# Kernel tuning notes

Measured on AMD Instinct MI355X. Metric: run time of the kernel, lower is better.

The kernel has to match this reference:

```python
import jax, jax.numpy as jnp
import numpy as np
import math

B, S, D_MODEL, H = 2, 2048, 1024, 16
D_HEAD = D_MODEL // H
THETA = 10000.0


def _init_linear(key, out_f, in_f):
    std = math.sqrt(2.0 / (out_f + in_f))
    w = jax.random.truncated_normal(key, -3.0, 3.0, (out_f, in_f), dtype=jnp.float32)
    return w * std


def setup_inputs() -> dict:
    key = jax.random.key(0)
    k1, k2, k3 = jax.random.split(key, 3)
    x = jax.random.normal(k1, (B, S, D_MODEL), dtype=jnp.float32)
    wqkv = _init_linear(k2, 3 * D_MODEL, D_MODEL)
    w_out = _init_linear(k3, D_MODEL, D_MODEL)
    # RoPE tables: positions [max_seq_len,1] * inv_freq [d_head//2]
    positions = jnp.arange(S, dtype=jnp.float32)[:, None]
    freqs = jnp.arange(0, D_HEAD, 2, dtype=jnp.float32) / D_HEAD
    inv_freq = 1.0 / (THETA ** freqs)
    angles = positions * inv_freq  # [S, D_HEAD//2]
    cos = jnp.cos(angles)
    sin = jnp.sin(angles)
    token_positions = jnp.arange(S, dtype=jnp.int32)
    return {"x": x, "wqkv": wqkv, "w_out": w_out, "cos": cos, "sin": sin,
            "token_positions": token_positions}


def _apply_rope(t, cos_pos, sin_pos):
    # t: [b, h, s, d], cos/sin_pos: [s, d//2] broadcast over b,h
    te = t[..., 0::2]
    to = t[..., 1::2]
    re = te * cos_pos - to * sin_pos
    ro = te * sin_pos + to * cos_pos
    # interleave even/odd back: [..., d//2, 2] -> [..., d]
    out = jnp.stack([re, ro], axis=-1)
    return out.reshape(t.shape)


def reference(x, wqkv, w_out, cos, sin, token_positions):
    b, s, d_model = x.shape
    qkv = jnp.einsum('oi,bsi->bso', wqkv, x)  # [b, s, 3*d_model]
    q, k, v = jnp.split(qkv, 3, axis=-1)

    def to_heads(t):
        return t.reshape(b, s, H, D_HEAD).transpose(0, 2, 1, 3)  # b h s d

    q, k, v = to_heads(q), to_heads(k), to_heads(v)

    cos_pos = cos[token_positions]  # [s, d_head//2]
    sin_pos = sin[token_positions]
    q = _apply_rope(q, cos_pos, sin_pos)
    k = _apply_rope(k, cos_pos, sin_pos)

    scores = jnp.einsum('bhqd,bhkd->bhqk', q, k) / math.sqrt(D_HEAD)
    causal = jnp.tril(jnp.ones((s, s), dtype=bool))  # ~triu(diag=1)
    scores = jnp.where(causal, scores, -jnp.inf)
    weights = jax.nn.softmax(scores, axis=-1)
    y = jnp.einsum('bhqk,bhkd->bhqd', weights, v)
    y = y.transpose(0, 2, 1, 3).reshape(b, s, d_model)
    return jnp.einsum('oi,bsi->bso', w_out, y)
```

## Files before the change

### kernel.cpp

```cpp
#include <hip/hip_runtime.h>
#include <hip/hip_bf16.h>


#define S_LEN 2048
#define DMODEL 1024
#define NH 16
#define QKVN 3072

typedef __attribute__((ext_vector_type(4))) short short4v;
typedef __attribute__((ext_vector_type(8))) short short8v;
typedef __attribute__((ext_vector_type(4))) float floatx4;

#define CSOFT 0.18033688f

__device__ __forceinline__ unsigned short f2bf(float f) {
  unsigned int u = __float_as_uint(f);
  u += 0x7FFFu + ((u >> 16) & 1u);
  return (unsigned short)(u >> 16);
}
__device__ __forceinline__ float bf2f(unsigned short u) {
  return __uint_as_float(((unsigned int)u) << 16);
}
__device__ __forceinline__ void gload16(const void* g, void* l) {
  __builtin_amdgcn_global_load_lds((const __attribute__((address_space(1))) void*)g,
                                   (__attribute__((address_space(3))) void*)l,
                                   16, 0, 0);
}
__device__ __forceinline__ int perm4(int c) {
  return (c >> 3) * 32 + (c & 3) * 8 + ((c >> 2) & 1) * 4;
}

__global__ __launch_bounds__(256) void cast_bf16_perm_k(const float* __restrict__ in,
                                                        unsigned short* __restrict__ out,
                                                        int nchunk) {
  int i = blockIdx.x * 256 + threadIdx.x;
  if (i >= nchunk) return;
  int c = i & 3;
  const float4* f4 = reinterpret_cast<const float4*>(in);
  float4 lo = f4[(i >> 2) * 8 + c];
  float4 hi = f4[(i >> 2) * 8 + 4 + c];
  short8v o;
  o[0] = (short)f2bf(lo.x); o[1] = (short)f2bf(lo.y);
  o[2] = (short)f2bf(lo.z); o[3] = (short)f2bf(lo.w);
  o[4] = (short)f2bf(hi.x); o[5] = (short)f2bf(hi.y);
  o[6] = (short)f2bf(hi.z); o[7] = (short)f2bf(hi.w);
  reinterpret_cast<short8v*>(out)[i] = o;
}

template <bool OUT_BF16>
__global__ __launch_bounds__(256) void gemm_bt(const unsigned short* __restrict__ A,
                                               const unsigned short* __restrict__ Bm,
                                               void* __restrict__ Cp, int M, int N, int K) {
  __shared__ __align__(16) unsigned short As[2][128 * 32];
  __shared__ __align__(16) unsigned short Bs[2][128 * 32];
  const int tid = threadIdx.x;
  const int lane = tid & 63;
  const int w = tid >> 6;
  const int wm = w >> 1, wn = w & 1;
  const int l15 = lane & 15, l4 = lane >> 4;
  const int bm = blockIdx.y * 128, bn = blockIdx.x * 128;
  const int srow = lane >> 2;
  const int schunk = ((lane & 3) - ((lane >> 3) & 3)) & 3;
  const int rslot = (l4 + (l15 >> 1)) & 3;

  floatx4 acc[4][4] = {};
  const int nt = K >> 5;

#define GSTAGE(T, BUF)                                                                   \
  {                                                                                      \
    const int k0s = (T) << 5;                                                            \
    _Pragma("unroll") for (int j = 0; j < 2; ++j) {                                      \
      const unsigned short* ga =                                                         \
          A + (size_t)(bm + j * 64 + w * 16 + srow) * K + k0s + schunk * 8;              \
      gload16(ga, &As[BUF][j * 2048 + w * 512]);                                         \
      const unsigned short* gb =                                                         \
          Bm + (size_t)(bn + j * 64 + w * 16 + srow) * K + k0s + schunk * 8;             \
      gload16(gb, &Bs[BUF][j * 2048 + w * 512]);                                         \
    }                                                                                    \
  }

  GSTAGE(0, 0);
  for (int t = 0; t < nt; ++t) {
    const int cur = t & 1;
    if (t + 1 < nt) {
      GSTAGE(t + 1, cur ^ 1);
      asm volatile("s_waitcnt vmcnt(4)" ::: "memory");
    } else {
      asm volatile("s_waitcnt vmcnt(0)" ::: "memory");
    }
    __syncthreads();

    short8v af[4], bfr[4];
#pragma unroll
    for (int f = 0; f < 4; ++f) {
      af[f]  = *(const short8v*)(&As[cur][(wm * 64 + f * 16 + l15) * 32 + rslot * 8]);
      bfr[f] = *(const short8v*)(&Bs[cur][(wn * 64 + f * 16 + l15) * 32 + rslot * 8]);
    }
#pragma unroll
    for (int f = 0; f < 4; ++f)
#pragma unroll
      for (int g = 0; g < 4; ++g)
        acc[f][g] = __builtin_amdgcn_mfma_f32_16x16x32_bf16(af[f], bfr[g], acc[f][g], 0, 0, 0);
    __syncthreads();
  }
#undef GSTAGE

#pragma unroll
  for (int f = 0; f < 4; ++f)
#pragma unroll
    for (int g = 0; g < 4; ++g)
#pragma unroll
      for (int r = 0; r < 4; ++r) {
        int row = bm + wm * 64 + f * 16 + l4 * 4 + r;
        int col = bn + wn * 64 + g * 16 + l15;
        if (OUT_BF16)
          ((unsigned short*)Cp)[(size_t)row * N + col] = f2bf(acc[f][g][r]);
        else
          ((float*)Cp)[(size_t)row * N + col] = acc[f][g][r];
      }
}

__global__ __launch_bounds__(256) void rope_pack_k(const unsigned short* __restrict__ qkvb,
                                                   unsigned short* __restrict__ qp_,
                                                   unsigned short* __restrict__ kp_,
                                                   unsigned short* __restrict__ vtp_,
                                                   const float* __restrict__ cosp,
                                                   const float* __restrict__ sinp,
                                                   const int* __restrict__ tpos) {
  __shared__ unsigned short Vs[64][68];
  const int tid = threadIdx.x;
  const int bh = blockIdx.x >> 5;
  const int st = blockIdx.x & 31;
  const int b = bh >> 4, h = bh & 15;
  const int c = tid & 15, t0 = tid >> 4;
  const int s0 = st * 64;
  const int pc = perm4(c);

#pragma unroll
  for (int it = 0; it < 4; ++it) {
    const int tl = it * 16 + t0;
    const int s = s0 + tl;
    const int tp = tpos[s];
    const size_t base = ((size_t)(b * S_LEN + s)) * QKVN + h * 64 + c * 4;
    const float co0 = cosp[tp * 32 + 2 * c], si0 = sinp[tp * 32 + 2 * c];
    const float co1 = cosp[tp * 32 + 2 * c + 1], si1 = sinp[tp * 32 + 2 * c + 1];
    {
      const float c0 = co0 * CSOFT, s0q = si0 * CSOFT;
      const float c1 = co1 * CSOFT, s1q = si1 * CSOFT;
      ushort4 rv = *(const ushort4*)(qkvb + base);
      float a0 = bf2f(rv.x), a1 = bf2f(rv.y), a2 = bf2f(rv.z), a3 = bf2f(rv.w);
      ushort4 ov;
      ov.x = f2bf(a0 * c0 - a1 * s0q); ov.y = f2bf(a0 * s0q + a1 * c0);
      ov.z = f2bf(a2 * c1 - a3 * s1q); ov.w = f2bf(a2 * s1q + a3 * c1);
      *(ushort4*)(qp_ + ((size_t)bh * S_LEN + s) * 64 + pc) = ov;
    }
    {
      ushort4 rv = *(const ushort4*)(qkvb + base + DMODEL);
      float a0 = bf2f(rv.x), a1 = bf2f(rv.y), a2 = bf2f(rv.z), a3 = bf2f(rv.w);
      ushort4 ov;
      ov.x = f2bf(a0 * co0 - a1 * si0); ov.y = f2bf(a0 * si0 + a1 * co0);
      ov.z = f2bf(a2 * co1 - a3 * si1); ov.w = f2bf(a2 * si1 + a3 * co1);
      *(ushort4*)(kp_ + ((size_t)bh * S_LEN + s) * 64 + pc) = ov;
    }
    {
      ushort4 rv = *(const ushort4*)(qkvb + base + 2 * DMODEL);
      *(ushort4*)(&Vs[tl][c * 4]) = rv;
    }
  }
  __syncthreads();
#pragma unroll
  for (int it = 0; it < 4; ++it) {
    const int d = it * 16 + t0;
    ushort4 ov;
    ov.x = Vs[c * 4 + 0][d]; ov.y = Vs[c * 4 + 1][d];
    ov.z = Vs[c * 4 + 2][d]; ov.w = Vs[c * 4 + 3][d];
    *(ushort4*)(vtp_ + ((size_t)bh * 64 + d) * S_LEN + s0 + pc) = ov;
  }
}

__device__ __forceinline__ short8v readfrag128(const unsigned short* L, int row, int cc) {
  return *(const short8v*)(L + row * 64 + (((cc) ^ (row & 7)) << 3));
}

__device__ __forceinline__ void stage_tiles(const unsigned short* kg0, const unsigned short* vg0,
                                            int kt, unsigned short* Kb, unsigned short* Vb,
                                            int tid, int w) {
#pragma unroll
  for (int i = 0; i < 2; ++i) {
    int jj = i * 256 + tid;
    int row = jj >> 3;
    int cc = (jj & 7) ^ (row & 7);
    gload16(kg0 + (size_t)kt * 4096 + row * 64 + cc * 8, Kb + (i * 256 + w * 64) * 8);
    gload16(vg0 + (size_t)row * S_LEN + kt * 64 + cc * 8, Vb + (i * 256 + w * 64) * 8);
  }
}

__global__ __launch_bounds__(256) void attn_mfma(const unsigned short* __restrict__ qp_,
                                                 const unsigned short* __restrict__ kp_,
                                                 const unsigned short* __restrict__ vtp_,
                                                 unsigned short* __restrict__ yb) {
  __shared__ __align__(16) unsigned short Kl[2][4096];
  __shared__ __align__(16) unsigned short Vl[2][4096];
  const int tid = threadIdx.x;
  const int lane = tid & 63, w = tid >> 6;
  const int l15 = lane & 15, l4 = lane >> 4;
  const int j = blockIdx.x;
  const int bh = (j & 7) + 8 * ((j >> 3) & 3);
  const int qt = 31 - (j >> 5);
  const int b = bh >> 4, h = bh & 15;

  const unsigned short* kg0 = kp_ + (size_t)bh * S_LEN * 64;
  const unsigned short* vg0 = vtp_ + (size_t)bh * 64 * S_LEN;

  const unsigned short* qp = qp_ + ((size_t)bh * S_LEN + qt * 64 + w * 16 + l15) * 64;
  short8v qf[2];
#pragma unroll
  for (int c2 = 0; c2 < 2; ++c2)
    qf[c2] = *(const short8v*)(qp + c2 * 32 + l4 * 8);

  floatx4 o[4] = {};
  float mrun = -1e30f, lsum = 0.f;

  stage_tiles(kg0, vg0, 0, Kl[0], Vl[0], tid, w);

  for (int kt = 0; kt <= qt; ++kt) {
    const int cur = kt & 1;
    if (kt < qt) {
      stage_tiles(kg0, vg0, kt + 1, Kl[cur ^ 1], Vl[cur ^ 1], tid, w);
      asm volatile("s_waitcnt vmcnt(4)" ::: "memory");
    } else {
      asm volatile("s_waitcnt vmcnt(0)" ::: "memory");
    }
    __syncthreads();

    const unsigned short* Kc = Kl[cur];
    const unsigned short* Vc = Vl[cur];
    const bool diag = (kt == qt);
    float s_[4][4];
    __builtin_amdgcn_s_setprio(1);
#pragma unroll
    for (int g = 0; g < 4; ++g) {
      if (diag && g > w) {
        s_[g][0] = s_[g][1] = s_[g][2] = s_[g][3] = -INFINITY;
        continue;
      }
      short8v k0 = readfrag128(Kc, g * 16 + l15, l4);
      short8v k1 = readfrag128(Kc, g * 16 + l15, 4 + l4);
      floatx4 t = {0.f, 0.f, 0.f, 0.f};
      t = __builtin_amdgcn_mfma_f32_16x16x32_bf16(k0, qf[0], t, 0, 0, 0);
      t = __builtin_amdgcn_mfma_f32_16x16x32_bf16(k1, qf[1], t, 0, 0, 0);
#pragma unroll
      for (int r = 0; r < 4; ++r) {
        float v = t[r];
        if (diag && g == w && (l4 * 4 + r > l15)) v = -INFINITY;
        s_[g][r] = v;
      }
    }
    __builtin_amdgcn_s_setprio(0);

    float tm = -INFINITY;
#pragma unroll
    for (int g = 0; g < 4; ++g)
#pragma unroll
      for (int r = 0; r < 4; ++r) tm = fmaxf(tm, s_[g][r]);
    tm = fmaxf(tm, __shfl_xor(tm, 16));
    tm = fmaxf(tm, __shfl_xor(tm, 32));

    if (!__all(tm <= mrun + 3.0f)) {
      float nm = fmaxf(mrun, tm);
      float rs = exp2f(mrun - nm);
      mrun = nm;
      lsum *= rs;
      float rsr[4];
#pragma unroll
      for (int r = 0; r < 4; ++r) rsr[r] = __shfl(rs, l4 * 4 + r);
#pragma unroll
      for (int dt = 0; dt < 4; ++dt)
#pragma unroll
        for (int r = 0; r < 4; ++r) o[dt][r] *= rsr[r];
    }

    union { unsigned short u[16]; short8v v[2]; } pk;
    float psum = 0.f;
#pragma unroll
    for (int g = 0; g < 4; ++g)
#pragma unroll
      for (int r = 0; r < 4; ++r) {
        float p = exp2f(s_[g][r] - mrun);
        psum += p;
        pk.u[g * 4 + r] = (unsigned short)(__float_as_uint(p) >> 16);
      }
    lsum += psum;

    __builtin_amdgcn_s_setprio(1);
#pragma unroll
    for (int dt = 0; dt < 4; ++dt) {
      short8v v0 = readfrag128(Vc, dt * 16 + l15, l4);
      short8v v1 = readfrag128(Vc, dt * 16 + l15, 4 + l4);
      o[dt] = __builtin_amdgcn_mfma_f32_16x16x32_bf16(pk.v[0], v0, o[dt], 0, 0, 0);
      o[dt] = __builtin_amdgcn_mfma_f32_16x16x32_bf16(pk.v[1], v1, o[dt], 0, 0, 0);
    }
    __builtin_amdgcn_s_setprio(0);
    __syncthreads();
  }

  lsum += __shfl_xor(lsum, 16);
  lsum += __shfl_xor(lsum, 32);
  float linv = 1.f / lsum;
  float lr[4];
#pragma unroll
  for (int r = 0; r < 4; ++r) lr[r] = __shfl(linv, l4 * 4 + r);
#pragma unroll
  for (int dt = 0; dt < 4; ++dt)
#pragma unroll
    for (int r = 0; r < 4; ++r) {
      size_t row = (size_t)(b * S_LEN + qt * 64 + w * 16 + l4 * 4 + r);
      int col = (h * 2 + (dt >> 1)) * 32 + (l15 >> 2) * 8 + (l15 & 3) + 4 * (dt & 1);
      yb[row * DMODEL + col] = f2bf(o[dt][r] * lr[r]);
    }
}

extern "C" void kernel_launch(void* const* d_in, const int* in_sizes, int n_in,
                              void* d_out, int out_size, void* d_ws, size_t ws_size,
                              hipStream_t stream) {
  const float* x     = (const float*)d_in[0];
  const float* wqkv  = (const float*)d_in[1];
  const float* w_out = (const float*)d_in[2];
  const float* cosp  = (const float*)d_in[3];
  const float* sinp  = (const float*)d_in[4];
  const int*   tpos  = (const int*)d_in[5];
  float* out = (float*)d_out;
  char* ws = (char*)d_ws;

  const size_t MB = 1024 * 1024;
  unsigned short* xb    = (unsigned short*)(ws + 0);
  unsigned short* wqkvb = (unsigned short*)(ws + 8 * MB);
  unsigned short* wob   = (unsigned short*)(ws + 14 * MB);
  unsigned short* qkvb  = (unsigned short*)(ws + 16 * MB);
  unsigned short* qpk   = (unsigned short*)(ws + 40 * MB);
  unsigned short* kpk   = (unsigned short*)(ws + 48 * MB);
  unsigned short* vtpk  = (unsigned short*)(ws + 56 * MB);
  unsigned short* yb    = (unsigned short*)(ws + 0);

  cast_bf16_perm_k<<<2048, 256, 0, stream>>>(x, xb, 524288);
  cast_bf16_perm_k<<<1536, 256, 0, stream>>>(wqkv, wqkvb, 393216);
  cast_bf16_perm_k<<<512, 256, 0, stream>>>(w_out, wob, 131072);

  gemm_bt<true><<<dim3(24, 32), 256, 0, stream>>>(xb, wqkvb, qkvb, 4096, QKVN, 1024);

  rope_pack_k<<<1024, 256, 0, stream>>>(qkvb, qpk, kpk, vtpk, cosp, sinp, tpos);

  attn_mfma<<<1024, 256, 0, stream>>>(qpk, kpk, vtpk, yb);

  gemm_bt<false><<<dim3(8, 32), 256, 0, stream>>>(yb, wob, out, 4096, DMODEL, 1024);
}
```

Measured before the change: 197.5 us.

## Unroll GEMM and attention loops by two, compute softmax row sums via MFMA

Both the GEMM main loop and the attention KV loop are manually unrolled by two, so the double-buffer index becomes a compile-time constant and the per-iteration buffer-select arithmetic goes away. In attention, the row sum of the probabilities is now produced by an MFMA against a ones vector rather than by scalar adds plus cross-lane shuffles. This sums the bf16-truncated probabilities, so the normaliser matches the values fed to the PV product. The rescale threshold is raised from 3 to 8, so the lazy rescale is skipped more often, at the cost of larger unnormalised accumulators. The GEMM unroll assumes an even K-tile count, which holds for K=1024.

New measurement: 198.1 us. About the same (+0.3%).

```diff
diff --git a/kernel.cpp b/kernel.cpp
--- a/kernel.cpp
+++ b/kernel.cpp
@@ -79,30 +79,32 @@
     }                                                                                    \
   }
 
+#define GBODY(T, BUF)                                                                    \
+  {                                                                                      \
+    if ((T) + 1 < nt) {                                                                  \
+      GSTAGE((T) + 1, BUF ^ 1);                                                          \
+      asm volatile("s_waitcnt vmcnt(4)" ::: "memory");                                   \
+    } else {                                                                             \
+      asm volatile("s_waitcnt vmcnt(0)" ::: "memory");                                   \
+    }                                                                                    \
+    __syncthreads();                                                                     \
+    short8v af[4], bfr[4];                                                               \
+    _Pragma("unroll") for (int f = 0; f < 4; ++f) {                                      \
+      af[f]  = *(const short8v*)(&As[BUF][(wm * 64 + f * 16 + l15) * 32 + rslot * 8]);   \
+      bfr[f] = *(const short8v*)(&Bs[BUF][(wn * 64 + f * 16 + l15) * 32 + rslot * 8]);   \
+    }                                                                                    \
+    _Pragma("unroll") for (int f = 0; f < 4; ++f)                                        \
+      _Pragma("unroll") for (int g = 0; g < 4; ++g)                                      \
+        acc[f][g] = __builtin_amdgcn_mfma_f32_16x16x32_bf16(af[f], bfr[g], acc[f][g], 0, 0, 0); \
+    __syncthreads();                                                                     \
+  }
+
   GSTAGE(0, 0);
-  for (int t = 0; t < nt; ++t) {
-    const int cur = t & 1;
-    if (t + 1 < nt) {
-      GSTAGE(t + 1, cur ^ 1);
-      asm volatile("s_waitcnt vmcnt(4)" ::: "memory");
-    } else {
-      asm volatile("s_waitcnt vmcnt(0)" ::: "memory");
-    }
-    __syncthreads();
-
-    short8v af[4], bfr[4];
-#pragma unroll
-    for (int f = 0; f < 4; ++f) {
-      af[f]  = *(const short8v*)(&As[cur][(wm * 64 + f * 16 + l15) * 32 + rslot * 8]);
-      bfr[f] = *(const short8v*)(&Bs[cur][(wn * 64 + f * 16 + l15) * 32 + rslot * 8]);
-    }
-#pragma unroll
-    for (int f = 0; f < 4; ++f)
-#pragma unroll
-      for (int g = 0; g < 4; ++g)
-        acc[f][g] = __builtin_amdgcn_mfma_f32_16x16x32_bf16(af[f], bfr[g], acc[f][g], 0, 0, 0);
-    __syncthreads();
-  }
+  for (int t = 0; t < nt; t += 2) {
+    GBODY(t, 0);
+    GBODY(t + 1, 1);
+  }
+#undef GBODY
 #undef GSTAGE
 
 #pragma unroll
@@ -218,105 +220,101 @@
   for (int c2 = 0; c2 < 2; ++c2)
     qf[c2] = *(const short8v*)(qp + c2 * 32 + l4 * 8);
 
+  const short8v ones8 = {(short)0x3F80, (short)0x3F80, (short)0x3F80, (short)0x3F80,
+                         (short)0x3F80, (short)0x3F80, (short)0x3F80, (short)0x3F80};
+
   floatx4 o[4] = {};
-  float mrun = -1e30f, lsum = 0.f;
+  floatx4 ls = {0.f, 0.f, 0.f, 0.f};
+  float mrun = -1e30f;
+
+#define ATTN_BODY(KT, BUF)                                                             \
+  {                                                                                    \
+    const int kt_ = (KT);                                                              \
+    if (kt_ < qt) {                                                                    \
+      stage_tiles(kg0, vg0, kt_ + 1, Kl[BUF ^ 1], Vl[BUF ^ 1], tid, w);                \
+      asm volatile("s_waitcnt vmcnt(4)" ::: "memory");                                 \
+    } else {                                                                           \
+      asm volatile("s_waitcnt vmcnt(0)" ::: "memory");                                 \
+    }                                                                                  \
+    __syncthreads();                                                                   \
+    const bool diag = (kt_ == qt);                                                     \
+    float s_[4][4];                                                                    \
+    __builtin_amdgcn_s_setprio(1);                                                     \
+    _Pragma("unroll") for (int g = 0; g < 4; ++g) {                                    \
+      if (diag && g > w) {                                                             \
+        s_[g][0] = s_[g][1] = s_[g][2] = s_[g][3] = -INFINITY;                         \
+        continue;                                                                      \
+      }                                                                                \
+      short8v k0 = readfrag128(Kl[BUF], g * 16 + l15, l4);                             \
+      short8v k1 = readfrag128(Kl[BUF], g * 16 + l15, 4 + l4);                         \
+      floatx4 t = {0.f, 0.f, 0.f, 0.f};                                                \
+      t = __builtin_amdgcn_mfma_f32_16x16x32_bf16(k0, qf[0], t, 0, 0, 0);              \
+      t = __builtin_amdgcn_mfma_f32_16x16x32_bf16(k1, qf[1], t, 0, 0, 0);              \
+      _Pragma("unroll") for (int r = 0; r < 4; ++r) {                                  \
+        float v = t[r];                                                                \
+        if (diag && g == w && (l4 * 4 + r > l15)) v = -INFINITY;                       \
+        s_[g][r] = v;                                                                  \
+      }                                                                                \
+    }                                                                                  \
+    __builtin_amdgcn_s_setprio(0);                                                     \
+    float tm = fmaxf(fmaxf(s_[0][0], s_[0][1]), s_[0][2]);                             \
+    tm = fmaxf(fmaxf(tm, s_[0][3]), s_[1][0]);                                         \
+    tm = fmaxf(fmaxf(tm, s_[1][1]), s_[1][2]);                                         \
+    tm = fmaxf(fmaxf(tm, s_[1][3]), s_[2][0]);                                         \
+    tm = fmaxf(fmaxf(tm, s_[2][1]), s_[2][2]);                                         \
+    tm = fmaxf(fmaxf(tm, s_[2][3]), s_[3][0]);                                         \
+    tm = fmaxf(fmaxf(tm, s_[3][1]), s_[3][2]);                                         \
+    tm = fmaxf(tm, s_[3][3]);                                                          \
+    tm = fmaxf(tm, __shfl_xor(tm, 16));                                                \
+    tm = fmaxf(tm, __shfl_xor(tm, 32));                                                \
+    if (!__all(tm <= mrun + 8.0f)) {                                                   \
+      float nm = fmaxf(mrun, tm);                                                      \
+      float rs = exp2f(mrun - nm);                                                     \
+      mrun = nm;                                                                       \
+      float rsr[4];                                                                    \
+      _Pragma("unroll") for (int r = 0; r < 4; ++r) rsr[r] = __shfl(rs, l4 * 4 + r);   \
+      _Pragma("unroll") for (int r = 0; r < 4; ++r) ls[r] *= rsr[r];                   \
+      _Pragma("unroll") for (int dt = 0; dt < 4; ++dt)                                 \
+        _Pragma("unroll") for (int r = 0; r < 4; ++r) o[dt][r] *= rsr[r];              \
+    }                                                                                  \
+    union { unsigned short u[16]; short8v v[2]; } pk;                                  \
+    _Pragma("unroll") for (int g = 0; g < 4; ++g)                                      \
+      _Pragma("unroll") for (int r = 0; r < 4; ++r) {                                  \
+        float p = exp2f(s_[g][r] - mrun);                                              \
+        pk.u[g * 4 + r] = (unsigned short)(__float_as_uint(p) >> 16);                  \
+      }                                                                                \
+    __builtin_amdgcn_s_setprio(1);                                                     \
+    ls = __builtin_amdgcn_mfma_f32_16x16x32_bf16(pk.v[0], ones8, ls, 0, 0, 0);         \
+    ls = __builtin_amdgcn_mfma_f32_16x16x32_bf16(pk.v[1], ones8, ls, 0, 0, 0);         \
+    _Pragma("unroll") for (int dt = 0; dt < 4; ++dt) {                                 \
+      short8v v0 = readfrag128(Vl[BUF], dt * 16 + l15, l4);                            \
+      short8v v1 = readfrag128(Vl[BUF], dt * 16 + l15, 4 + l4);                        \
+      o[dt] = __builtin_amdgcn_mfma_f32_16x16x32_bf16(pk.v[0], v0, o[dt], 0, 0, 0);    \
+      o[dt] = __builtin_amdgcn_mfma_f32_16x16x32_bf16(pk.v[1], v1, o[dt], 0, 0, 0);    \
+    }                                                                                  \
+    __builtin_amdgcn_s_setprio(0);                                                     \
+    __syncthreads();                                                                   \
+  }
 
   stage_tiles(kg0, vg0, 0, Kl[0], Vl[0], tid, w);
-
-  for (int kt = 0; kt <= qt; ++kt) {
-    const int cur = kt & 1;
-    if (kt < qt) {
-      stage_tiles(kg0, vg0, kt + 1, Kl[cur ^ 1], Vl[cur ^ 1], tid, w);
-      asm volatile("s_waitcnt vmcnt(4)" ::: "memory");
-    } else {
-      asm volatile("s_waitcnt vmcnt(0)" ::: "memory");
-    }
-    __syncthreads();
-
-    const unsigned short* Kc = Kl[cur];
-    const unsigned short* Vc = Vl[cur];
-    const bool diag = (kt == qt);
-    float s_[4][4];
-    __builtin_amdgcn_s_setprio(1);
-#pragma unroll
-    for (int g = 0; g < 4; ++g) {
-      if (diag && g > w) {
-        s_[g][0] = s_[g][1] = s_[g][2] = s_[g][3] = -INFINITY;
-        continue;
-      }
-      short8v k0 = readfrag128(Kc, g * 16 + l15, l4);
-      short8v k1 = readfrag128(Kc, g * 16 + l15, 4 + l4);
-      floatx4 t = {0.f, 0.f, 0.f, 0.f};
-      t = __builtin_amdgcn_mfma_f32_16x16x32_bf16(k0, qf[0], t, 0, 0, 0);
-      t = __builtin_amdgcn_mfma_f32_16x16x32_bf16(k1, qf[1], t, 0, 0, 0);
-#pragma unroll
-      for (int r = 0; r < 4; ++r) {
-        float v = t[r];
-        if (diag && g == w && (l4 * 4 + r > l15)) v = -INFINITY;
-        s_[g][r] = v;
-      }
-    }
-    __builtin_amdgcn_s_setprio(0);
-
-    float tm = -INFINITY;
-#pragma unroll
-    for (int g = 0; g < 4; ++g)
-#pragma unroll
-      for (int r = 0; r < 4; ++r) tm = fmaxf(tm, s_[g][r]);
-    tm = fmaxf(tm, __shfl_xor(tm, 16));
-    tm = fmaxf(tm, __shfl_xor(tm, 32));
-
-    if (!__all(tm <= mrun + 3.0f)) {
-      float nm = fmaxf(mrun, tm);
-      float rs = exp2f(mrun - nm);
-      mrun = nm;
-      lsum *= rs;
-      float rsr[4];
-#pragma unroll
-      for (int r = 0; r < 4; ++r) rsr[r] = __shfl(rs, l4 * 4 + r);
-#pragma unroll
-      for (int dt = 0; dt < 4; ++dt)
-#pragma unroll
-        for (int r = 0; r < 4; ++r) o[dt][r] *= rsr[r];
-    }
-
-    union { unsigned short u[16]; short8v v[2]; } pk;
-    float psum = 0.f;
-#pragma unroll
-    for (int g = 0; g < 4; ++g)
-#pragma unroll
-      for (int r = 0; r < 4; ++r) {
-        float p = exp2f(s_[g][r] - mrun);
-        psum += p;
-        pk.u[g * 4 + r] = (unsigned short)(__float_as_uint(p) >> 16);
-      }
-    lsum += psum;
-
-    __builtin_amdgcn_s_setprio(1);
-#pragma unroll
-    for (int dt = 0; dt < 4; ++dt) {
-      short8v v0 = readfrag128(Vc, dt * 16 + l15, l4);
-      short8v v1 = readfrag128(Vc, dt * 16 + l15, 4 + l4);
-      o[dt] = __builtin_amdgcn_mfma_f32_16x16x32_bf16(pk.v[0], v0, o[dt], 0, 0, 0);
-      o[dt] = __builtin_amdgcn_mfma_f32_16x16x32_bf16(pk.v[1], v1, o[dt], 0, 0, 0);
-    }
-    __builtin_amdgcn_s_setprio(0);
-    __syncthreads();
-  }
-
-  lsum += __shfl_xor(lsum, 16);
-  lsum += __shfl_xor(lsum, 32);
-  float linv = 1.f / lsum;
-  float lr[4];
-#pragma unroll
-  for (int r = 0; r < 4; ++r) lr[r] = __shfl(linv, l4 * 4 + r);
+  int kt = 0;
+  for (; kt + 1 <= qt; kt += 2) {
+    ATTN_BODY(kt, 0);
+    ATTN_BODY(kt + 1, 1);
+  }
+  if (kt <= qt) ATTN_BODY(kt, 0);
+#undef ATTN_BODY
+
+  float linv[4];
+#pragma unroll
+  for (int r = 0; r < 4; ++r) linv[r] = 1.f / ls[r];
 #pragma unroll
   for (int dt = 0; dt < 4; ++dt)
 #pragma unroll
     for (int r = 0; r < 4; ++r) {
       size_t row = (size_t)(b * S_LEN + qt * 64 + w * 16 + l4 * 4 + r);
       int col = (h * 2 + (dt >> 1)) * 32 + (l15 >> 2) * 8 + (l15 & 3) + 4 * (dt & 1);
-      yb[row * DMODEL + col] = f2bf(o[dt][r] * lr[r]);
+      yb[row * DMODEL + col] = f2bf(o[dt][r] * linv[r]);
     }
 }
 
```
